# Optimization experiments

Measured on AMD Instinct MI355X. Metric: run time of the kernel, lower is better.

The kernel has to match this reference:

```python
import jax, jax.numpy as jnp
import numpy as np

H_DIM = 1024
NUM_HEADS = 16
HEAD_DIM = H_DIM // NUM_HEADS
EPS = 1e-5


def rms_norm(x, w, eps=EPS):
    var = jnp.mean(jnp.square(x), axis=-1, keepdims=True)
    return x * jax.lax.rsqrt(var + eps) * w


def setup_inputs() -> dict:
    key = jax.random.key(0)
    ks = jax.random.split(key, 8)
    B, S = 2, 2048
    x = jax.random.normal(ks[0], (B, S, H_DIM), dtype=jnp.float32)
    # learned params (orthogonal init approximated by scaled normal for a correctness baseline)
    qkv_w = jax.random.normal(ks[1], (3 * H_DIM, H_DIM), dtype=jnp.float32) / np.sqrt(H_DIM)
    gate_w = jax.random.normal(ks[2], (NUM_HEADS, H_DIM), dtype=jnp.float32) / np.sqrt(H_DIM)
    o_w = jax.random.normal(ks[3], (H_DIM, H_DIM), dtype=jnp.float32) / np.sqrt(H_DIM)
    prenorm_w = jnp.ones((H_DIM,), dtype=jnp.float32)
    q_norm_w = jnp.ones((HEAD_DIM,), dtype=jnp.float32)
    k_norm_w = jnp.ones((HEAD_DIM,), dtype=jnp.float32)
    return {"x": x, "prenorm_w": prenorm_w, "qkv_w": qkv_w, "gate_w": gate_w,
            "o_w": o_w, "q_norm_w": q_norm_w, "k_norm_w": k_norm_w}


def reference(x, prenorm_w, qkv_w, gate_w, o_w, q_norm_w, k_norm_w):
    B, S, D = x.shape
    residual = x
    xn = rms_norm(x, prenorm_w)                                   # [B,S,D]
    qkv = jnp.einsum('bsd,ed->bse', xn, qkv_w)                    # [B,S,3D]
    qkv = qkv.reshape(B, S, 3, NUM_HEADS, HEAD_DIM)
    gate = jnp.einsum('bsd,hd->bsh', xn, gate_w)                  # [B,S,H]
    q, k, v = qkv[:, :, 0], qkv[:, :, 1], qkv[:, :, 2]            # [B,S,H,hd]
    q = rms_norm(q, q_norm_w)
    k = rms_norm(k, k_norm_w)
    scale = 1.0 / np.sqrt(HEAD_DIM).astype(np.float32)
    scores = jnp.einsum('bqhd,bkhd->bhqk', q, k) * scale          # [B,H,S,S]
    attn = jax.nn.softmax(scores, axis=-1)
    out = jnp.einsum('bhqk,bkhd->bhqd', attn, v)                  # [B,H,S,hd]
    out = out * jax.nn.sigmoid(gate).transpose(0, 2, 1)[..., None]
    out = out.transpose(0, 2, 1, 3).reshape(B, S, D)              # [B,S,D]
    return jnp.einsum('bsd,ed->bse', out, o_w) + residual
```

## Files before the change

kernel.cpp:

```cpp
#include <hip/hip_runtime.h>
#include <math.h>

typedef __bf16 bf16x8 __attribute__((ext_vector_type(8)));
typedef float f32x4 __attribute__((ext_vector_type(4)));
typedef float f32x16 __attribute__((ext_vector_type(16)));
typedef unsigned int uint2v __attribute__((ext_vector_type(2)));
typedef unsigned int uint4v __attribute__((ext_vector_type(4)));
typedef unsigned short ushort_t;

#define SEQ 2048
#define MROWS 4096
#define EPS 1e-5f
#define QKS 3200
#define LOG2E 1.4426950408889634f
#define SMAX_B2 17.32f

__device__ __forceinline__ float bf2f(ushort_t u) {
  union { unsigned int i; float f; } c; c.i = ((unsigned int)u) << 16; return c.f;
}
__device__ __forceinline__ ushort_t f2bf(float f) {
  union { unsigned int i; float f; } c; c.f = f;
  unsigned int i = c.i;
  unsigned int r = i + 0x7fffu + ((i >> 16) & 1u);
  return (ushort_t)(r >> 16);
}
__device__ __forceinline__ ushort_t f2bf_fast(float f) {
  union { __bf16 b; ushort_t u; } cv; cv.b = (__bf16)f; return cv.u;
}

__device__ __forceinline__ float exp2_raw(float x) {
  float r; asm("v_exp_f32 %0, %1" : "=v"(r) : "v"(x)); return r;
}

#define CVTPK(d, a, b) asm("v_cvt_pk_bf16_f32 %0, %1, %2" : "=v"(d) : "v"(a), "v"(b))

__device__ __forceinline__ void plane_swap(unsigned int &a, unsigned int &b) {
#if __has_builtin(__builtin_amdgcn_permlane32_swap)
  uint2v r = __builtin_amdgcn_permlane32_swap(a, b, 0, 0);
  a = r.x; b = r.y;
#else
  unsigned int sa = (unsigned int)__shfl_xor((int)a, 32);
  unsigned int sb = (unsigned int)__shfl_xor((int)b, 32);
  int hi = (int)((threadIdx.x & 63) >> 5);
  unsigned int na = hi ? sb : a;
  unsigned int nb = hi ? b : sa;
  a = na; b = nb;
#endif
}

__device__ __forceinline__ void softmax_pack(const f32x16 &stv, float &lp,
                                             uint4v &Fa, uint4v &Fb) {
  float p[16];
  #pragma unroll
  for (int r = 0; r < 16; ++r) p[r] = exp2_raw(stv[r] - SMAX_B2);
  float s0 = (p[0] + p[1]) + (p[2] + p[3]);
  float s1 = (p[4] + p[5]) + (p[6] + p[7]);
  float s2 = (p[8] + p[9]) + (p[10] + p[11]);
  float s3 = (p[12] + p[13]) + (p[14] + p[15]);
  lp += (s0 + s1) + (s2 + s3);
  unsigned int X00, X01, X10, X11, X20, X21, X30, X31;
  CVTPK(X00, p[0], p[1]);   CVTPK(X01, p[2], p[3]);
  CVTPK(X10, p[4], p[5]);   CVTPK(X11, p[6], p[7]);
  CVTPK(X20, p[8], p[9]);   CVTPK(X21, p[10], p[11]);
  CVTPK(X30, p[12], p[13]); CVTPK(X31, p[14], p[15]);
  plane_swap(X00, X10); plane_swap(X01, X11);
  plane_swap(X20, X30); plane_swap(X21, X31);
  Fa.x = X00; Fa.y = X01; Fa.z = X10; Fa.w = X11;
  Fb.x = X20; Fb.y = X21; Fb.z = X30; Fb.w = X31;
}

__device__ __forceinline__ float wave_sum(float v) {
  #pragma unroll
  for (int off = 32; off > 0; off >>= 1) v += __shfl_xor(v, off);
  return v;
}

__global__ void detect_kernel(const unsigned int* __restrict__ xraw, int* __restrict__ flag) {
  int tid = threadIdx.x;
  int cnt = 0;
  for (int i = tid; i < 4096; i += 256) {
    unsigned int e = (xraw[i] >> 7) & 0xFFu;
    cnt += (e >= 100u && e <= 150u) ? 1 : 0;
  }
  __shared__ int sred[256];
  sred[tid] = cnt;
  __syncthreads();
  for (int s = 128; s > 0; s >>= 1) {
    if (tid < s) sred[tid] += sred[tid + s];
    __syncthreads();
  }
  if (tid == 0) flag[0] = (sred[0] > 2048) ? 1 : 0;
}

__global__ void prep_kernel(const void* __restrict__ qkvw_in, const void* __restrict__ gw_in,
                            const void* __restrict__ ow_in, const void* __restrict__ pw_in,
                            const void* __restrict__ qn_in, const void* __restrict__ kn_in,
                            ushort_t* __restrict__ Wcat, ushort_t* __restrict__ ow,
                            float* __restrict__ pwf, float* __restrict__ qnf,
                            float* __restrict__ knf, const int* __restrict__ flag) {
  int bid = blockIdx.x, tid = threadIdx.x;
  int bf = *flag;
  if (bid < 3072) {
    long long i4 = (long long)bid * 256 + tid;
    if (bf) {
      ((ushort4*)Wcat)[i4] = ((const ushort4*)qkvw_in)[i4];
    } else {
      float4 f = ((const float4*)qkvw_in)[i4];
      ushort4 o;
      o.x = f2bf(f.x); o.y = f2bf(f.y); o.z = f2bf(f.z); o.w = f2bf(f.w);
      ((ushort4*)Wcat)[i4] = o;
    }
  } else if (bid < 3088) {
    long long j4 = (long long)(bid - 3072) * 256 + tid;
    ushort4* dst = (ushort4*)(Wcat + 3072 * 1024);
    if (bf) {
      dst[j4] = ((const ushort4*)gw_in)[j4];
    } else {
      float4 f = ((const float4*)gw_in)[j4];
      ushort4 o;
      o.x = f2bf(f.x); o.y = f2bf(f.y); o.z = f2bf(f.z); o.w = f2bf(f.w);
      dst[j4] = o;
    }
  } else if (bid < 4112) {
    long long j4 = (long long)(bid - 3088) * 256 + tid;
    if (bf) {
      ((ushort4*)ow)[j4] = ((const ushort4*)ow_in)[j4];
    } else {
      float4 f = ((const float4*)ow_in)[j4];
      ushort4 o;
      o.x = f2bf(f.x); o.y = f2bf(f.y); o.z = f2bf(f.z); o.w = f2bf(f.w);
      ((ushort4*)ow)[j4] = o;
    }
  } else {
    for (int i = tid; i < 1024; i += 256)
      pwf[i] = bf ? bf2f(((const ushort_t*)pw_in)[i]) : ((const float*)pw_in)[i];
    if (tid < 64) {
      qnf[tid] = bf ? bf2f(((const ushort_t*)qn_in)[tid]) : ((const float*)qn_in)[tid];
      knf[tid] = bf ? bf2f(((const ushort_t*)kn_in)[tid]) : ((const float*)kn_in)[tid];
    }
  }
}

__global__ void prenorm_kernel(const void* __restrict__ xraw,
                               const float* __restrict__ w,
                               ushort_t* __restrict__ xn,
                               const int* __restrict__ flag) {
  int row = blockIdx.x;
  int tid = threadIdx.x;
  float4 u;
  if (*flag) {
    ushort4 s = ((const ushort4*)xraw)[row * 256 + tid];
    u.x = bf2f(s.x); u.y = bf2f(s.y); u.z = bf2f(s.z); u.w = bf2f(s.w);
  } else {
    u = ((const float4*)xraw)[row * 256 + tid];
  }
  float ss = u.x*u.x + u.y*u.y + u.z*u.z + u.w*u.w;
  ss = wave_sum(ss);
  __shared__ float red[4];
  if ((tid & 63) == 0) red[tid >> 6] = ss;
  __syncthreads();
  float total = red[0] + red[1] + red[2] + red[3];
  float inv = rsqrtf(total * (1.0f / 1024.0f) + EPS);
  float4 wu = ((const float4*)w)[tid];
  ushort4 o;
  o.x = f2bf(u.x * inv * wu.x);
  o.y = f2bf(u.y * inv * wu.y);
  o.z = f2bf(u.z * inv * wu.z);
  o.w = f2bf(u.w * inv * wu.w);
  ((ushort4*)(xn + (long long)row * 1024))[tid] = o;
}

__device__ __forceinline__ void gll16(const ushort_t* g, ushort_t* l) {
  __builtin_amdgcn_global_load_lds(
      (const __attribute__((address_space(1))) unsigned int*)g,
      (__attribute__((address_space(3))) unsigned int*)l, 16, 0, 0);
}

__global__ void gemm_qkv_fused(const ushort_t* __restrict__ A, const ushort_t* __restrict__ B,
                               ushort_t* __restrict__ C, float* __restrict__ gate,
                               ushort_t* __restrict__ Vt,
                               const float* __restrict__ qw, const float* __restrict__ kw) {
  __shared__ char gsm[128 * 136 * 2] __attribute__((aligned(16)));
  ushort_t* As = (ushort_t*)gsm;
  ushort_t* Bs = (ushort_t*)(gsm + 8192);
  int tid = threadIdx.x, wave = tid >> 6, lane = tid & 63;
  int lin = blockIdx.x;
  int xcd = lin & 7;
  int i2 = lin >> 3;
  int my = (xcd << 2) + i2 / 25;
  int nx = i2 % 25;
  int m_blk = my * 128, n_blk = nx * 128;
  int wm = (wave & 1) * 64, wn = (wave >> 1) * 64;
  int g = lane >> 4, c = lane & 15;
  int arow = lane >> 2;
  int akc = (lane & 3) << 3;
  f32x4 acc[4][4] = {};
  for (int kt = 0; kt < 1024; kt += 32) {
    #pragma unroll
    for (int i = 0; i < 2; ++i) {
      int rbase = (i * 4 + wave) * 16;
      gll16(A + (long long)(m_blk + rbase + arow) * 1024 + kt + akc, &As[rbase * 32]);
      gll16(B + (long long)(n_blk + rbase + arow) * 1024 + kt + akc, &Bs[rbase * 32]);
    }
    __syncthreads();
    bf16x8 af[4], bfr[4];
    #pragma unroll
    for (int mi = 0; mi < 4; ++mi)
      af[mi] = *(const bf16x8*)&As[(wm + mi * 16 + c) * 32 + (g << 3)];
    #pragma unroll
    for (int ni = 0; ni < 4; ++ni)
      bfr[ni] = *(const bf16x8*)&Bs[(wn + ni * 16 + c) * 32 + (g << 3)];
    #pragma unroll
    for (int mi = 0; mi < 4; ++mi)
      #pragma unroll
      for (int ni = 0; ni < 4; ++ni)
        acc[mi][ni] = __builtin_amdgcn_mfma_f32_16x16x32_bf16(af[mi], bfr[ni], acc[mi][ni], 0, 0, 0);
    __syncthreads();
  }
  int col_base = n_blk + wn;
  if (col_base < 2048) {
    int isk = col_base >= 1024;
    float scale = isk ? 1.0f : (0.125f * LOG2E);
    const float* nw = isk ? kw : qw;
    float w[4];
    #pragma unroll
    for (int ni = 0; ni < 4; ++ni) w[ni] = nw[ni * 16 + c];
    #pragma unroll
    for (int mi = 0; mi < 4; ++mi)
      #pragma unroll
      for (int r = 0; r < 4; ++r) {
        float ss = 0.f;
        #pragma unroll
        for (int ni = 0; ni < 4; ++ni) ss += acc[mi][ni][r] * acc[mi][ni][r];
        #pragma unroll
        for (int off = 8; off > 0; off >>= 1) ss += __shfl_xor(ss, off);
        float inv = rsqrtf(ss * (1.0f / 64.0f) + EPS) * scale;
        int row = m_blk + wm + mi * 16 + g * 4 + r;
        #pragma unroll
        for (int ni = 0; ni < 4; ++ni)
          C[(long long)row * QKS + col_base + ni * 16 + c] = f2bf(acc[mi][ni][r] * inv * w[ni]);
      }
  } else if (n_blk < 3072) {
    ushort_t* vts = (ushort_t*)gsm;
    const int VSTR = 136;
    #pragma unroll
    for (int mi = 0; mi < 4; ++mi)
      #pragma unroll
      for (int r = 0; r < 4; ++r) {
        int row_l = wm + mi * 16 + g * 4 + r;
        #pragma unroll
        for (int ni = 0; ni < 4; ++ni) {
          int col_l = wn + ni * 16 + c;
          vts[col_l * VSTR + row_l] = f2bf(acc[mi][ni][r]);
        }
      }
    __syncthreads();
    int rowv = tid >> 1, half = tid & 1;
    int vcol = (n_blk - 2048) + rowv;
    int h = vcol >> 6, d = vcol & 63;
    int b2 = m_blk >> 11;
    ushort_t* dst = Vt + ((long long)(b2 * 16 + h) * 64 + d) * SEQ + (m_blk & 2047) + half * 64;
    const ushort_t* srcl = &vts[rowv * VSTR + half * 64];
    #pragma unroll
    for (int j = 0; j < 8; ++j)
      *(bf16x8*)(dst + j * 8) = *(const bf16x8*)(srcl + j * 8);
  } else if (col_base == 3072) {
    #pragma unroll
    for (int mi = 0; mi < 4; ++mi)
      #pragma unroll
      for (int r = 0; r < 4; ++r) {
        int row = m_blk + wm + mi * 16 + g * 4 + r;
        float v = acc[mi][0][r];
        gate[(long long)row * 16 + c] = 1.0f / (1.0f + __expf(-v));
      }
  }
}

__global__ void gemm_tiled(const ushort_t* __restrict__ A, const ushort_t* __restrict__ B,
                           void* __restrict__ Cv, const void* __restrict__ res,
                           const int* __restrict__ flag,
                           int K, int lda, int ldb, int ldc) {
  __shared__ ushort_t As[128 * 32];
  __shared__ ushort_t Bs[128 * 32];
  int tid = threadIdx.x, wave = tid >> 6, lane = tid & 63;
  int lin = blockIdx.x;
  int xcd = lin & 7;
  int i2 = lin >> 3;
  int my = (xcd << 2) + (i2 >> 3);
  int nx = i2 & 7;
  int m_blk = my * 128, n_blk = nx * 128;
  int wm = (wave & 1) * 64, wn = (wave >> 1) * 64;
  int g = lane >> 4, c = lane & 15;
  int arow = lane >> 2;
  int akc = (lane & 3) << 3;
  f32x4 acc[4][4] = {};
  for (int kt = 0; kt < K; kt += 32) {
    #pragma unroll
    for (int i = 0; i < 2; ++i) {
      int rbase = (i * 4 + wave) * 16;
      gll16(A + (long long)(m_blk + rbase + arow) * lda + kt + akc, &As[rbase * 32]);
      gll16(B + (long long)(n_blk + rbase + arow) * ldb + kt + akc, &Bs[rbase * 32]);
    }
    __syncthreads();
    bf16x8 af[4], bfr[4];
    #pragma unroll
    for (int mi = 0; mi < 4; ++mi)
      af[mi] = *(const bf16x8*)&As[(wm + mi * 16 + c) * 32 + (g << 3)];
    #pragma unroll
    for (int ni = 0; ni < 4; ++ni)
      bfr[ni] = *(const bf16x8*)&Bs[(wn + ni * 16 + c) * 32 + (g << 3)];
    #pragma unroll
    for (int mi = 0; mi < 4; ++mi)
      #pragma unroll
      for (int ni = 0; ni < 4; ++ni)
        acc[mi][ni] = __builtin_amdgcn_mfma_f32_16x16x32_bf16(af[mi], bfr[ni], acc[mi][ni], 0, 0, 0);
    __syncthreads();
  }
  int outbf = flag ? *flag : 1;
  #pragma unroll
  for (int mi = 0; mi < 4; ++mi)
    #pragma unroll
    for (int ni = 0; ni < 4; ++ni)
      #pragma unroll
      for (int r = 0; r < 4; ++r) {
        int row = m_blk + wm + mi * 16 + g * 4 + r;
        int col = n_blk + wn + ni * 16 + c;
        long long idx = (long long)row * ldc + col;
        float v = acc[mi][ni][r];
        if (res) v += outbf ? bf2f(((const ushort_t*)res)[idx]) : ((const float*)res)[idx];
        if (outbf) ((ushort_t*)Cv)[idx] = f2bf(v);
        else       ((float*)Cv)[idx] = v;
      }
}

__global__ __launch_bounds__(256, 4)
void flash_kernel(const ushort_t* __restrict__ qkv, const ushort_t* __restrict__ Vt,
                  const float* __restrict__ gate, ushort_t* __restrict__ ao) {
  __shared__ char smem[32768] __attribute__((aligned(16)));
  ushort_t* KsB = (ushort_t*)smem;
  ushort_t* VsB = (ushort_t*)(smem + 16384);
  int tid = threadIdx.x, wave = tid >> 6, lane = tid & 63;
  int al = lane & 31, hi = lane >> 5;
  int fal = (al & 7) ^ ((al >> 3) & 3);
  int qh = wave & 1, kh = wave >> 1;
  int khb = kh * 32;
  int bid = blockIdx.x;
  int xcd = bid & 7, idx = bid >> 3;
  int bh = (xcd << 2) | (idx >> 5);
  int q0 = (idx & 31) * 64;
  int b = bh >> 4, h = bh & 15;
  const ushort_t* qbase = qkv + (long long)b * SEQ * QKS + h * 64;
  const ushort_t* kbase = qbase + 1024;
  const ushort_t* vtbase = Vt + (long long)bh * 64 * SEQ;
  int qrow = q0 + qh * 32 + al;
  bf16x8 bq0 = *(const bf16x8*)(qbase + (long long)qrow * QKS + 0 * 16 + hi * 8);
  bf16x8 bq1 = *(const bf16x8*)(qbase + (long long)qrow * QKS + 1 * 16 + hi * 8);
  bf16x8 bq2 = *(const bf16x8*)(qbase + (long long)qrow * QKS + 2 * 16 + hi * 8);
  bf16x8 bq3 = *(const bf16x8*)(qbase + (long long)qrow * QKS + 3 * 16 + hi * 8);
  asm volatile("s_waitcnt vmcnt(0)"
               :
               : "v"(__builtin_bit_cast(f32x4, bq0)), "v"(__builtin_bit_cast(f32x4, bq1)),
                 "v"(__builtin_bit_cast(f32x4, bq2)), "v"(__builtin_bit_cast(f32x4, bq3))
               : "memory");
  f32x16 oac0 = {}, oac1 = {};
  float lp = 0.f;
  int srow = lane >> 3;
  int schk = lane & 7;

  #define STAGE(BUF, S0) do {                                                        \
    int gch = ((schk ^ srow ^ wave) & 7) << 3;                                       \
    int lbo = (BUF) * 4096;                                                          \
    _Pragma("unroll")                                                                \
    for (int tt = 0; tt < 2; ++tt) {                                                 \
      int rb = tt * 32 + wave * 8;                                                   \
      int row = rb + srow;                                                           \
      gll16(kbase + (long long)((S0) + row) * QKS + gch, &KsB[lbo + rb * 64]);       \
      gll16(vtbase + (long long)row * SEQ + (S0) + gch, &VsB[lbo + rb * 64]);        \
    } } while (0)

  #define PIPE_BAR(N) do {                                                           \
    asm volatile("s_waitcnt vmcnt(" #N ")" ::: "memory");                            \
    __builtin_amdgcn_s_barrier();                                                    \
    asm volatile("" ::: "memory");                                                   \
  } while (0)

  #define COMPUTE(BUF) do {                                                          \
    int lbo = (BUF) * 4096;                                                          \
    f32x16 st = {};                                                                  \
    __builtin_amdgcn_s_setprio(1);                                                   \
    _Pragma("unroll")                                                                \
    for (int dst = 0; dst < 4; ++dst) {                                              \
      int ph = (((dst << 1) | hi) ^ fal) << 3;                                       \
      bf16x8 ak = *(const bf16x8*)&KsB[lbo + (khb + al) * 64 + ph];                  \
      bf16x8 qq = (dst == 0) ? bq0 : (dst == 1) ? bq1 : (dst == 2) ? bq2 : bq3;      \
      st = __builtin_amdgcn_mfma_f32_32x32x16_bf16(ak, qq, st, 0, 0, 0);             \
    }                                                                                \
    __builtin_amdgcn_s_setprio(0);                                                   \
    uint4v Fa, Fb;                                                                   \
    softmax_pack(st, lp, Fa, Fb);                                                    \
    bf16x8 pf0 = __builtin_bit_cast(bf16x8, Fa);                                     \
    bf16x8 pf1 = __builtin_bit_cast(bf16x8, Fb);                                     \
    __builtin_amdgcn_s_setprio(1);                                                   \
    _Pragma("unroll")                                                                \
    for (int kst = 0; kst < 2; ++kst) {                                              \
      int kg = kh * 2 + kst;                                                         \
      int ph = (((kg << 1) | hi) ^ fal) << 3;                                        \
      bf16x8 av0 = *(const bf16x8*)&VsB[lbo + al * 64 + ph];                         \
      bf16x8 av1 = *(const bf16x8*)&VsB[lbo + (32 + al) * 64 + ph];                  \
      bf16x8 pf = kst ? pf1 : pf0;                                                   \
      oac0 = __builtin_amdgcn_mfma_f32_32x32x16_bf16(av0, pf, oac0, 0, 0, 0);        \
      oac1 = __builtin_amdgcn_mfma_f32_32x32x16_bf16(av1, pf, oac1, 0, 0, 0);        \
    }                                                                                \
    __builtin_amdgcn_s_setprio(0);                                                   \
  } while (0)

  STAGE(0, 0);
  for (int it = 0; it < 31; ++it) {
    STAGE((it + 1) & 1, (it + 1) * 64);
    PIPE_BAR(4);
    COMPUTE(it & 1);
    __builtin_amdgcn_s_barrier();
  }
  PIPE_BAR(0);
  COMPUTE(1);
  #undef STAGE
  #undef PIPE_BAR
  #undef COMPUTE

  float ltot = lp + __shfl_xor(lp, 32);
  float* cbuf = (float*)smem;
  float* lbuf = cbuf + 64 * 65;
  int qrl = qh * 32 + al;
  __syncthreads();
  if (kh == 1) {
    #pragma unroll
    for (int r = 0; r < 16; ++r) {
      int d = (r & 3) + 8 * (r >> 2) + 4 * hi;
      cbuf[qrl * 65 + d]      = oac0[r];
      cbuf[qrl * 65 + 32 + d] = oac1[r];
    }
    if (hi == 0) lbuf[qrl] = ltot;
  }
  __syncthreads();
  if (kh == 0) {
    ltot += lbuf[qrl];
    #pragma unroll
    for (int r = 0; r < 16; ++r) {
      int d = (r & 3) + 8 * (r >> 2) + 4 * hi;
      oac0[r] += cbuf[qrl * 65 + d];
      oac1[r] += cbuf[qrl * 65 + 32 + d];
    }
    float sg = gate[(long long)(b * SEQ + qrow) * 16 + h];
    float scale = sg / ltot;
    ushort_t* aobase = ao + (long long)(b * SEQ + qrow) * 1024 + h * 64;
    #define OSTORE(OA, MT) do {                                                      \
      _Pragma("unroll")                                                              \
      for (int tt = 0; tt < 4; ++tt) {                                               \
        ushort4 o;                                                                   \
        o.x = f2bf_fast(OA[4 * tt + 0] * scale);                                     \
        o.y = f2bf_fast(OA[4 * tt + 1] * scale);                                     \
        o.z = f2bf_fast(OA[4 * tt + 2] * scale);                                     \
        o.w = f2bf_fast(OA[4 * tt + 3] * scale);                                     \
        *(ushort4*)(aobase + (MT) * 32 + 8 * tt + 4 * hi) = o;                       \
      } } while (0)
    OSTORE(oac0, 0);
    OSTORE(oac1, 1);
    #undef OSTORE
  }
}

extern "C" void kernel_launch(void* const* d_in, const int* in_sizes, int n_in,
                              void* d_out, int out_size, void* d_ws, size_t ws_size,
                              hipStream_t stream) {
  (void)in_sizes; (void)n_in; (void)out_size; (void)ws_size;
  char* ws = (char*)d_ws;
  ushort_t* Wcat = (ushort_t*)(ws);
  ushort_t* ow   = (ushort_t*)(ws + (7ll << 20));
  float*    pwf  = (float*)   (ws + (9ll << 20));
  float*    qnf  = (float*)   (ws + (9ll << 20) + (8 << 10));
  float*    knf  = (float*)   (ws + (9ll << 20) + (12 << 10));
  int*      flag = (int*)     (ws + (9ll << 20) + (16 << 10));
  float*    gate = (float*)   (ws + (9ll << 20) + (64 << 10));
  ushort_t* xn   = (ushort_t*)(ws + (10ll << 20));
  ushort_t* qkv2 = (ushort_t*)(ws + (18ll << 20));
  ushort_t* Vt   = (ushort_t*)(ws + (44ll << 20));
  ushort_t* ao   = (ushort_t*)(ws + (52ll << 20));

  detect_kernel<<<1, 256, 0, stream>>>((const unsigned int*)d_in[0], flag);
  prep_kernel<<<4113, 256, 0, stream>>>(d_in[2], d_in[3], d_in[4], d_in[1], d_in[5], d_in[6],
                                        Wcat, ow, pwf, qnf, knf, flag);
  prenorm_kernel<<<MROWS, 256, 0, stream>>>(d_in[0], pwf, xn, flag);
  gemm_qkv_fused<<<dim3(800), 256, 0, stream>>>(xn, Wcat, qkv2, gate, Vt, qnf, knf);
  flash_kernel<<<dim3(1024), 256, 0, stream>>>(qkv2, Vt, gate, ao);
  gemm_tiled<<<dim3(256), 256, 0, stream>>>(ao, ow, d_out, d_in[0], flag,
                                            1024, 1024, 1024, 1024);
}
```

Before: 223.6 us.

## Fuse weight prep with prenorm and deepen GEMM K-step to 64

Merges the weight-conversion kernel and the RMS prenorm kernel into one launch, with the prenorm reading the norm weight directly from the input instead of a staged fp32 copy. Both GEMM kernels now load two 32-wide K slices per barrier pair, halving the number of __syncthreads per tile. The aim is to cut one kernel launch plus the barrier overhead in the GEMM main loops, at the cost of doubled LDS per block, which may lower occupancy.

```diff
diff --git a/kernel.cpp b/kernel.cpp
--- a/kernel.cpp
+++ b/kernel.cpp
@@ -92,12 +92,15 @@
   if (tid == 0) flag[0] = (sred[0] > 2048) ? 1 : 0;
 }
 
-__global__ void prep_kernel(const void* __restrict__ qkvw_in, const void* __restrict__ gw_in,
-                            const void* __restrict__ ow_in, const void* __restrict__ pw_in,
-                            const void* __restrict__ qn_in, const void* __restrict__ kn_in,
-                            ushort_t* __restrict__ Wcat, ushort_t* __restrict__ ow,
-                            float* __restrict__ pwf, float* __restrict__ qnf,
-                            float* __restrict__ knf, const int* __restrict__ flag) {
+__global__ void prep_norm_kernel(const void* __restrict__ qkvw_in, const void* __restrict__ gw_in,
+                                 const void* __restrict__ ow_in, const void* __restrict__ pw_in,
+                                 const void* __restrict__ qn_in, const void* __restrict__ kn_in,
+                                 const void* __restrict__ xraw,
+                                 ushort_t* __restrict__ Wcat, ushort_t* __restrict__ ow,
+                                 float* __restrict__ qnf, float* __restrict__ knf,
+                                 ushort_t* __restrict__ xn,
+                                 const int* __restrict__ flag) {
+  __shared__ float red[4];
   int bid = blockIdx.x, tid = threadIdx.x;
   int bf = *flag;
   if (bid < 3072) {
@@ -131,43 +134,40 @@
       o.x = f2bf(f.x); o.y = f2bf(f.y); o.z = f2bf(f.z); o.w = f2bf(f.w);
       ((ushort4*)ow)[j4] = o;
     }
-  } else {
-    for (int i = tid; i < 1024; i += 256)
-      pwf[i] = bf ? bf2f(((const ushort_t*)pw_in)[i]) : ((const float*)pw_in)[i];
+  } else if (bid == 4112) {
     if (tid < 64) {
       qnf[tid] = bf ? bf2f(((const ushort_t*)qn_in)[tid]) : ((const float*)qn_in)[tid];
       knf[tid] = bf ? bf2f(((const ushort_t*)kn_in)[tid]) : ((const float*)kn_in)[tid];
     }
-  }
-}
-
-__global__ void prenorm_kernel(const void* __restrict__ xraw,
-                               const float* __restrict__ w,
-                               ushort_t* __restrict__ xn,
-                               const int* __restrict__ flag) {
-  int row = blockIdx.x;
-  int tid = threadIdx.x;
-  float4 u;
-  if (*flag) {
-    ushort4 s = ((const ushort4*)xraw)[row * 256 + tid];
-    u.x = bf2f(s.x); u.y = bf2f(s.y); u.z = bf2f(s.z); u.w = bf2f(s.w);
   } else {
-    u = ((const float4*)xraw)[row * 256 + tid];
-  }
-  float ss = u.x*u.x + u.y*u.y + u.z*u.z + u.w*u.w;
-  ss = wave_sum(ss);
-  __shared__ float red[4];
-  if ((tid & 63) == 0) red[tid >> 6] = ss;
-  __syncthreads();
-  float total = red[0] + red[1] + red[2] + red[3];
-  float inv = rsqrtf(total * (1.0f / 1024.0f) + EPS);
-  float4 wu = ((const float4*)w)[tid];
-  ushort4 o;
-  o.x = f2bf(u.x * inv * wu.x);
-  o.y = f2bf(u.y * inv * wu.y);
-  o.z = f2bf(u.z * inv * wu.z);
-  o.w = f2bf(u.w * inv * wu.w);
-  ((ushort4*)(xn + (long long)row * 1024))[tid] = o;
+    int row = bid - 4113;
+    float4 u;
+    if (bf) {
+      ushort4 s = ((const ushort4*)xraw)[row * 256 + tid];
+      u.x = bf2f(s.x); u.y = bf2f(s.y); u.z = bf2f(s.z); u.w = bf2f(s.w);
+    } else {
+      u = ((const float4*)xraw)[row * 256 + tid];
+    }
+    float ss = u.x*u.x + u.y*u.y + u.z*u.z + u.w*u.w;
+    ss = wave_sum(ss);
+    if ((tid & 63) == 0) red[tid >> 6] = ss;
+    __syncthreads();
+    float total = red[0] + red[1] + red[2] + red[3];
+    float inv = rsqrtf(total * (1.0f / 1024.0f) + EPS);
+    float4 wu;
+    if (bf) {
+      ushort4 s = ((const ushort4*)pw_in)[tid];
+      wu.x = bf2f(s.x); wu.y = bf2f(s.y); wu.z = bf2f(s.z); wu.w = bf2f(s.w);
+    } else {
+      wu = ((const float4*)pw_in)[tid];
+    }
+    ushort4 o;
+    o.x = f2bf(u.x * inv * wu.x);
+    o.y = f2bf(u.y * inv * wu.y);
+    o.z = f2bf(u.z * inv * wu.z);
+    o.w = f2bf(u.w * inv * wu.w);
+    ((ushort4*)(xn + (long long)row * 1024))[tid] = o;
+  }
 }
 
 __device__ __forceinline__ void gll16(const ushort_t* g, ushort_t* l) {
@@ -182,7 +182,7 @@
                                const float* __restrict__ qw, const float* __restrict__ kw) {
   __shared__ char gsm[128 * 136 * 2] __attribute__((aligned(16)));
   ushort_t* As = (ushort_t*)gsm;
-  ushort_t* Bs = (ushort_t*)(gsm + 8192);
+  ushort_t* Bs = (ushort_t*)(gsm + 16384);
   int tid = threadIdx.x, wave = tid >> 6, lane = tid & 63;
   int lin = blockIdx.x;
   int xcd = lin & 7;
@@ -195,26 +195,33 @@
   int arow = lane >> 2;
   int akc = (lane & 3) << 3;
   f32x4 acc[4][4] = {};
-  for (int kt = 0; kt < 1024; kt += 32) {
-    #pragma unroll
-    for (int i = 0; i < 2; ++i) {
-      int rbase = (i * 4 + wave) * 16;
-      gll16(A + (long long)(m_blk + rbase + arow) * 1024 + kt + akc, &As[rbase * 32]);
-      gll16(B + (long long)(n_blk + rbase + arow) * 1024 + kt + akc, &Bs[rbase * 32]);
-    }
-    __syncthreads();
-    bf16x8 af[4], bfr[4];
-    #pragma unroll
-    for (int mi = 0; mi < 4; ++mi)
-      af[mi] = *(const bf16x8*)&As[(wm + mi * 16 + c) * 32 + (g << 3)];
-    #pragma unroll
-    for (int ni = 0; ni < 4; ++ni)
-      bfr[ni] = *(const bf16x8*)&Bs[(wn + ni * 16 + c) * 32 + (g << 3)];
-    #pragma unroll
-    for (int mi = 0; mi < 4; ++mi)
+  for (int kt = 0; kt < 1024; kt += 64) {
+    #pragma unroll
+    for (int hh = 0; hh < 2; ++hh)
+      #pragma unroll
+      for (int i = 0; i < 2; ++i) {
+        int rbase = (i * 4 + wave) * 16;
+        gll16(A + (long long)(m_blk + rbase + arow) * 1024 + kt + hh * 32 + akc,
+              &As[hh * 4096 + rbase * 32]);
+        gll16(B + (long long)(n_blk + rbase + arow) * 1024 + kt + hh * 32 + akc,
+              &Bs[hh * 4096 + rbase * 32]);
+      }
+    __syncthreads();
+    #pragma unroll
+    for (int hh = 0; hh < 2; ++hh) {
+      bf16x8 af[4], bfr[4];
+      #pragma unroll
+      for (int mi = 0; mi < 4; ++mi)
+        af[mi] = *(const bf16x8*)&As[hh * 4096 + (wm + mi * 16 + c) * 32 + (g << 3)];
       #pragma unroll
       for (int ni = 0; ni < 4; ++ni)
-        acc[mi][ni] = __builtin_amdgcn_mfma_f32_16x16x32_bf16(af[mi], bfr[ni], acc[mi][ni], 0, 0, 0);
+        bfr[ni] = *(const bf16x8*)&Bs[hh * 4096 + (wn + ni * 16 + c) * 32 + (g << 3)];
+      #pragma unroll
+      for (int mi = 0; mi < 4; ++mi)
+        #pragma unroll
+        for (int ni = 0; ni < 4; ++ni)
+          acc[mi][ni] = __builtin_amdgcn_mfma_f32_16x16x32_bf16(af[mi], bfr[ni], acc[mi][ni], 0, 0, 0);
+    }
     __syncthreads();
   }
   int col_base = n_blk + wn;
@@ -280,8 +287,8 @@
                            void* __restrict__ Cv, const void* __restrict__ res,
                            const int* __restrict__ flag,
                            int K, int lda, int ldb, int ldc) {
-  __shared__ ushort_t As[128 * 32];
-  __shared__ ushort_t Bs[128 * 32];
+  __shared__ ushort_t As[2 * 128 * 32];
+  __shared__ ushort_t Bs[2 * 128 * 32];
   int tid = threadIdx.x, wave = tid >> 6, lane = tid & 63;
   int lin = blockIdx.x;
   int xcd = lin & 7;
@@ -294,26 +301,33 @@
   int arow = lane >> 2;
   int akc = (lane & 3) << 3;
   f32x4 acc[4][4] = {};
-  for (int kt = 0; kt < K; kt += 32) {
-    #pragma unroll
-    for (int i = 0; i < 2; ++i) {
-      int rbase = (i * 4 + wave) * 16;
-      gll16(A + (long long)(m_blk + rbase + arow) * lda + kt + akc, &As[rbase * 32]);
-      gll16(B + (long long)(n_blk + rbase + arow) * ldb + kt + akc, &Bs[rbase * 32]);
-    }
-    __syncthreads();
-    bf16x8 af[4], bfr[4];
-    #pragma unroll
-    for (int mi = 0; mi < 4; ++mi)
-      af[mi] = *(const bf16x8*)&As[(wm + mi * 16 + c) * 32 + (g << 3)];
-    #pragma unroll
-    for (int ni = 0; ni < 4; ++ni)
-      bfr[ni] = *(const bf16x8*)&Bs[(wn + ni * 16 + c) * 32 + (g << 3)];
-    #pragma unroll
-    for (int mi = 0; mi < 4; ++mi)
+  for (int kt = 0; kt < K; kt += 64) {
+    #pragma unroll
+    for (int hh = 0; hh < 2; ++hh)
+      #pragma unroll
+      for (int i = 0; i < 2; ++i) {
+        int rbase = (i * 4 + wave) * 16;
+        gll16(A + (long long)(m_blk + rbase + arow) * lda + kt + hh * 32 + akc,
+              &As[hh * 4096 + rbase * 32]);
+        gll16(B + (long long)(n_blk + rbase + arow) * ldb + kt + hh * 32 + akc,
+              &Bs[hh * 4096 + rbase * 32]);
+      }
+    __syncthreads();
+    #pragma unroll
+    for (int hh = 0; hh < 2; ++hh) {
+      bf16x8 af[4], bfr[4];
+      #pragma unroll
+      for (int mi = 0; mi < 4; ++mi)
+        af[mi] = *(const bf16x8*)&As[hh * 4096 + (wm + mi * 16 + c) * 32 + (g << 3)];
       #pragma unroll
       for (int ni = 0; ni < 4; ++ni)
-        acc[mi][ni] = __builtin_amdgcn_mfma_f32_16x16x32_bf16(af[mi], bfr[ni], acc[mi][ni], 0, 0, 0);
+        bfr[ni] = *(const bf16x8*)&Bs[hh * 4096 + (wn + ni * 16 + c) * 32 + (g << 3)];
+      #pragma unroll
+      for (int mi = 0; mi < 4; ++mi)
+        #pragma unroll
+        for (int ni = 0; ni < 4; ++ni)
+          acc[mi][ni] = __builtin_amdgcn_mfma_f32_16x16x32_bf16(af[mi], bfr[ni], acc[mi][ni], 0, 0, 0);
+    }
     __syncthreads();
   }
   int outbf = flag ? *flag : 1;
@@ -476,7 +490,6 @@
   char* ws = (char*)d_ws;
   ushort_t* Wcat = (ushort_t*)(ws);
   ushort_t* ow   = (ushort_t*)(ws + (7ll << 20));
-  float*    pwf  = (float*)   (ws + (9ll << 20));
   float*    qnf  = (float*)   (ws + (9ll << 20) + (8 << 10));
   float*    knf  = (float*)   (ws + (9ll << 20) + (12 << 10));
   int*      flag = (int*)     (ws + (9ll << 20) + (16 << 10));
@@ -487,9 +500,8 @@
   ushort_t* ao   = (ushort_t*)(ws + (52ll << 20));
 
   detect_kernel<<<1, 256, 0, stream>>>((const unsigned int*)d_in[0], flag);
-  prep_kernel<<<4113, 256, 0, stream>>>(d_in[2], d_in[3], d_in[4], d_in[1], d_in[5], d_in[6],
-                                        Wcat, ow, pwf, qnf, knf, flag);
-  prenorm_kernel<<<MROWS, 256, 0, stream>>>(d_in[0], pwf, xn, flag);
+  prep_norm_kernel<<<8209, 256, 0, stream>>>(d_in[2], d_in[3], d_in[4], d_in[1], d_in[5], d_in[6],
+                                             d_in[0], Wcat, ow, qnf, knf, xn, flag);
   gemm_qkv_fused<<<dim3(800), 256, 0, stream>>>(xn, Wcat, qkv2, gate, Vt, qnf, knf);
   flash_kernel<<<dim3(1024), 256, 0, stream>>>(qkv2, Vt, gate, ao);
   gemm_tiled<<<dim3(256), 256, 0, stream>>>(ao, ow, d_out, d_in[0], flag,
```

Result: faster. 218.4 us (-2.4%).
